# Optimization experiments

Hardware: AMD Instinct MI355X
Metric: run time of the kernel (lower is better)

Reference implementation:

```python
import jax, jax.numpy as jnp
import numpy as np

N = 50000      # nodes
E = 600000     # edges (no self-loops in data; GATConv adds them)
IN = 128       # input_dim
HID = 16       # hidden_dim
H1 = 8         # heads1
H2 = 4         # heads2
OUT = 40       # output_dim (classes)
EPS_BN = 1e-5
NEG_SLOPE = 0.2


def setup_inputs() -> dict:
    key = jax.random.key(0)
    ks = jax.random.split(key, 40)
    f32 = jnp.float32

    def p(k, shape, scale=0.1):
        return (jax.random.normal(k, shape) * scale).astype(f32)

    x = jax.random.normal(ks[0], (N, IN), f32)
    src = jax.random.randint(ks[1], (E,), 0, N)
    off = jax.random.randint(ks[2], (E,), 1, N)
    dst = (src + off) % N  # guarantees src != dst
    edge_index = jnp.stack([src, dst]).astype(jnp.int32)

    D1 = HID * H1  # 128
    D2 = HID * H2  # 64
    inp = {
        "x": x, "edge_index": edge_index,
        # conv1: IN -> HID per head, H1 heads, concat
        "W1": p(ks[3], (IN, H1 * HID)), "as1": p(ks[4], (H1, HID)), "ad1": p(ks[5], (H1, HID)), "b1": p(ks[6], (D1,)),
        "g1": jnp.ones((D1,), f32), "be1": jnp.zeros((D1,), f32),
        # conv_mid: D1 -> D1, 1 head, mean (concat=False)
        "Wm": p(ks[7], (D1, D1)), "asm": p(ks[8], (1, D1)), "adm": p(ks[9], (1, D1)), "bm": p(ks[10], (D1,)),
        "gm": jnp.ones((D1,), f32), "bem": jnp.zeros((D1,), f32),
        # conv2: D1 -> HID per head, H2 heads, concat
        "W2": p(ks[11], (D1, H2 * HID)), "as2": p(ks[12], (H2, HID)), "ad2": p(ks[13], (H2, HID)), "b2": p(ks[14], (D2,)),
        "g2": jnp.ones((D2,), f32), "be2": jnp.zeros((D2,), f32),
        # conv3: D2 -> OUT, 1 head, mean
        "W3": p(ks[15], (D2, OUT)), "as3": p(ks[16], (1, OUT)), "ad3": p(ks[17], (1, OUT)), "b3": p(ks[18], (OUT,)),
        "g3": jnp.ones((OUT,), f32), "be3": jnp.zeros((OUT,), f32),
    }
    return inp


def _gat(x, src, dst, W, a_s, a_d, b, concat):
    """PyG GATConv forward (self-loops already appended to src/dst)."""
    Nn = x.shape[0]
    H, C = a_s.shape
    h = (x @ W).reshape(Nn, H, C)                       # [N,H,C]
    s = (h * a_s).sum(-1)                               # [N,H] source score
    d = (h * a_d).sum(-1)                               # [N,H] dest score
    e = jax.nn.leaky_relu(s[src] + d[dst], NEG_SLOPE)   # [E,H]
    # segment softmax over incoming edges of each dst node
    m = jax.ops.segment_max(e, dst, num_segments=Nn)    # [N,H]
    ee = jnp.exp(e - m[dst])
    den = jax.ops.segment_sum(ee, dst, num_segments=Nn)
    alpha = ee / (den[dst] + 1e-16)                     # [E,H]
    out = jax.ops.segment_sum(h[src] * alpha[:, :, None], dst, num_segments=Nn)  # [N,H,C]
    out = out.reshape(Nn, H * C) if concat else out.mean(axis=1)
    return out + b


def _bn(x, g, b):
    mu = x.mean(axis=0)
    var = x.var(axis=0)
    return g * (x - mu) * jax.lax.rsqrt(var + EPS_BN) + b


def reference(x, edge_index, W1, as1, ad1, b1, g1, be1, Wm, asm, adm, bm, gm, bem,
              W2, as2, ad2, b2, g2, be2, W3, as3, ad3, b3, g3, be3):
    Nn = x.shape[0]
    loops = jnp.arange(Nn, dtype=edge_index.dtype)
    src = jnp.concatenate([edge_index[0], loops])
    dst = jnp.concatenate([edge_index[1], loops])

    h = jax.nn.elu(_bn(_gat(x, src, dst, W1, as1, ad1, b1, True), g1, be1))
    res = h
    h = jax.nn.elu(_bn(_gat(h, src, dst, Wm, asm, adm, bm, False), gm, bem))
    h = res + h
    h = jax.nn.elu(_bn(_gat(h, src, dst, W2, as2, ad2, b2, True), g2, be2))
    h = _bn(_gat(h, src, dst, W3, as3, ad3, b3, False), g3, be3)
    return jax.nn.log_softmax(h, axis=1)
```

## Files before the change

kernel.cpp:

```cpp
#include <hip/hip_runtime.h>
#include <hip/hip_bf16.h>
#include <math.h>

#define NN 50000
#define NE 600000
#define ET (NN + NE)

typedef __hip_bfloat16 bf16;

__global__ void k_hist(const int* __restrict__ ei, int* __restrict__ deg) {
    int e = blockIdx.x * blockDim.x + threadIdx.x;
    if (e >= ET) return;
    int d = (e < NE) ? ei[NE + e] : (e - NE);
    atomicAdd(&deg[d], 1);
}

__global__ void k_scan_local(const int* __restrict__ deg, int* __restrict__ tmp,
                             int* __restrict__ csum) {
    __shared__ int wsum[16];
    int i = blockIdx.x * 1024 + threadIdx.x;
    int lane = threadIdx.x & 63, wid = threadIdx.x >> 6;
    int x = (i < NN) ? deg[i] : 0;
    for (int off = 1; off < 64; off <<= 1) {
        int y = __shfl_up(x, off);
        if (lane >= off) x += y;
    }
    if (lane == 63) wsum[wid] = x;
    __syncthreads();
    if (wid == 0) {
        int t = (lane < 16) ? wsum[lane] : 0;
        for (int off = 1; off < 16; off <<= 1) {
            int y = __shfl_up(t, off);
            if (lane >= off) t += y;
        }
        if (lane < 16) wsum[lane] = t;
    }
    __syncthreads();
    if (wid > 0) x += wsum[wid - 1];
    if (i < NN) tmp[i] = x;
    if (threadIdx.x == 1023) csum[blockIdx.x] = x;
}

__global__ void k_scan_chunks(int* __restrict__ csum, int nchunks) {
    int lane = threadIdx.x;
    int v = (lane < nchunks) ? csum[lane] : 0;
    for (int off = 1; off < 64; off <<= 1) {
        int y = __shfl_up(v, off);
        if (lane >= off) v += y;
    }
    if (lane < nchunks) csum[lane] = v;
}

__global__ void k_rowptr(const int* __restrict__ tmp, const int* __restrict__ csum,
                         int* __restrict__ rowptr) {
    int i = blockIdx.x * blockDim.x + threadIdx.x;
    if (i == 0) rowptr[0] = 0;
    if (i < NN) {
        int chunk = i >> 10;
        int off = (chunk > 0) ? csum[chunk - 1] : 0;
        rowptr[i + 1] = tmp[i] + off;
    }
}

__global__ void k_fill(const int* __restrict__ ei, const int* __restrict__ rowptr,
                       int* __restrict__ fill, int* __restrict__ csr) {
    int e = blockIdx.x * blockDim.x + threadIdx.x;
    if (e >= ET) return;
    int s = (e < NE) ? ei[e] : (e - NE);
    int d = (e < NE) ? ei[NE + e] : (e - NE);
    int pos = atomicAdd(&fill[d], 1);
    csr[rowptr[d] + pos] = s;
}

template <int K, int D, bool FS1>
__global__ __launch_bounds__(256) void k_gemm(const float* __restrict__ X,
                                              const float* __restrict__ W,
                                              bf16* __restrict__ Hout, int nrows,
                                              const float* __restrict__ a_s,
                                              const float* __restrict__ a_d,
                                              float* __restrict__ Sout,
                                              float* __restrict__ Dvout) {
    __shared__ float Xs[64][K + 1];
    int t = threadIdx.x;
    int row0 = blockIdx.x * 64;
    for (int i = t; i < 64 * K; i += 256) {
        int r = i / K, c = i % K;
        int gr = row0 + r;
        Xs[r][c] = (gr < nrows) ? X[(size_t)gr * K + c] : 0.f;
    }
    __syncthreads();
    constexpr int DC = D / 32;
    int tx = t & 31, ty = t >> 5;
    float acc[8][DC];
#pragma unroll
    for (int r = 0; r < 8; r++)
#pragma unroll
        for (int c = 0; c < DC; c++) acc[r][c] = 0.f;
    for (int k = 0; k < K; k++) {
        float w[DC];
#pragma unroll
        for (int c = 0; c < DC; c++) w[c] = W[k * D + tx + 32 * c];
#pragma unroll
        for (int r = 0; r < 8; r++) {
            float xv = Xs[ty * 8 + r][k];
#pragma unroll
            for (int c = 0; c < DC; c++) acc[r][c] += xv * w[c];
        }
    }
#pragma unroll
    for (int r = 0; r < 8; r++) {
        int gr = row0 + ty * 8 + r;
        if (gr < nrows)
#pragma unroll
            for (int c = 0; c < DC; c++)
                Hout[(size_t)gr * D + tx + 32 * c] = __float2bfloat16(acc[r][c]);
    }
    if constexpr (FS1) {
        float asv[DC], adv[DC];
#pragma unroll
        for (int c = 0; c < DC; c++) {
            asv[c] = a_s[tx + 32 * c];
            adv[c] = a_d[tx + 32 * c];
        }
#pragma unroll
        for (int r = 0; r < 8; r++) {
            float sa = 0.f, da = 0.f;
#pragma unroll
            for (int c = 0; c < DC; c++) {
                sa += acc[r][c] * asv[c];
                da += acc[r][c] * adv[c];
            }
            for (int off = 16; off; off >>= 1) {
                sa += __shfl_xor(sa, off);
                da += __shfl_xor(da, off);
            }
            int gr = row0 + ty * 8 + r;
            if (tx == 0 && gr < nrows) {
                Sout[gr] = sa;
                Dvout[gr] = da;
            }
        }
    }
}

__global__ void k_gemm_small(const float* __restrict__ X, const float* __restrict__ W,
                             bf16* __restrict__ Hout, const float* __restrict__ a_s,
                             const float* __restrict__ a_d, float* __restrict__ S,
                             float* __restrict__ Dv) {
    __shared__ float xs[64];
    int n = blockIdx.x, t = threadIdx.x;
    xs[t] = X[n * 64 + t];
    __syncthreads();
    float acc = 0.f;
    if (t < 40) {
#pragma unroll
        for (int k = 0; k < 64; k++) acc += xs[k] * W[k * 40 + t];
        Hout[n * 40 + t] = __float2bfloat16(acc);
    }
    float sa = (t < 40) ? acc * a_s[t] : 0.f;
    float da = (t < 40) ? acc * a_d[t] : 0.f;
    for (int off = 32; off; off >>= 1) {
        sa += __shfl_xor(sa, off);
        da += __shfl_xor(da, off);
    }
    if (t == 0) {
        S[n] = sa;
        Dv[n] = da;
    }
}

template <int H, int C>
__global__ void k_scores(const bf16* __restrict__ Hb, const float* __restrict__ a_s,
                         const float* __restrict__ a_d, float* __restrict__ S,
                         float* __restrict__ Dv) {
    int t = blockIdx.x * blockDim.x + threadIdx.x;
    if (t >= NN * H) return;
    int n = t / H, h = t % H;
    const bf16* base = Hb + (size_t)n * (H * C) + h * C;
    float sa = 0.f, da = 0.f;
#pragma unroll
    for (int c = 0; c < C; c++) {
        float v = __bfloat162float(base[c]);
        sa += v * a_s[h * C + c];
        da += v * a_d[h * C + c];
    }
    S[t] = sa;
    Dv[t] = da;
}

template <int H, int C, int D>
__global__ __launch_bounds__(256) void k_aggregate(const bf16* __restrict__ Hb,
                                                   const float* __restrict__ S,
                                                   const float* __restrict__ Dv,
                                                   const int* __restrict__ rowptr,
                                                   const int* __restrict__ csr,
                                                   float* __restrict__ Out) {
    constexpr int WCAP = 64;
    __shared__ float wl[4][WCAP * H];
    int nl = threadIdx.x >> 6;
    int node = blockIdx.x * 4 + nl;
    if (node >= NN) return;
    int lane = threadIdx.x & 63;
    int r0 = rowptr[node], r1 = rowptr[node + 1];
    int cnt = r1 - r0;
    float dn[H], den[H];
#pragma unroll
    for (int h = 0; h < H; h++) {
        dn[h] = Dv[node * H + h];
        den[h] = 0.f;
    }
    for (int k = lane; k < cnt; k += 64) {
        int u = csr[r0 + k];
        float sv[H];
        if constexpr (H == 8) {
            float4 s0 = *reinterpret_cast<const float4*>(S + (size_t)u * 8);
            float4 s1 = *reinterpret_cast<const float4*>(S + (size_t)u * 8 + 4);
            sv[0] = s0.x; sv[1] = s0.y; sv[2] = s0.z; sv[3] = s0.w;
            sv[4] = s1.x; sv[5] = s1.y; sv[6] = s1.z; sv[7] = s1.w;
        } else if constexpr (H == 4) {
            float4 s0 = *reinterpret_cast<const float4*>(S + (size_t)u * 4);
            sv[0] = s0.x; sv[1] = s0.y; sv[2] = s0.z; sv[3] = s0.w;
        } else {
            sv[0] = S[u];
        }
        float ex[H];
#pragma unroll
        for (int h = 0; h < H; h++) {
            float e = sv[h] + dn[h];
            e = fmaxf(e, 0.2f * e);
            ex[h] = __expf(e);
            den[h] += ex[h];
        }
        if (k < WCAP) {
#pragma unroll
            for (int h = 0; h < H; h++) wl[nl][k * H + h] = ex[h];
        }
    }
#pragma unroll
    for (int h = 0; h < H; h++) {
        for (int off = 32; off; off >>= 1) den[h] += __shfl_xor(den[h], off);
        den[h] = 1.f / (den[h] + 1e-16f);
    }

    constexpr int EPI = (D > 64) ? 1 : 2;
    constexpr int LP = 64 / EPI;
    int sub = lane / LP;
    int j = lane % LP;
    bool act = (2 * j) < D;
    const int h_l = act ? (2 * j) / C : 0;
    float dninv_l = den[0], dn_l = dn[0];
#pragma unroll
    for (int h = 1; h < H; h++) {
        dninv_l = (h_l == h) ? den[h] : dninv_l;
        dn_l = (h_l == h) ? dn[h] : dn_l;
    }
    const float* wlp = &wl[nl][0];
    auto wof = [&](int idx, int u) -> float {
        if (idx < WCAP) return wlp[idx * H + h_l];
        float e = S[(size_t)u * H + h_l] + dn_l;
        e = fmaxf(e, 0.2f * e);
        return __expf(e);
    };
    float ax = 0.f, ay = 0.f;
    int k = sub;
    for (; k + 3 * EPI < cnt; k += 4 * EPI) {
        int u0 = csr[r0 + k];
        int u1 = csr[r0 + k + EPI];
        int u2 = csr[r0 + k + 2 * EPI];
        int u3 = csr[r0 + k + 3 * EPI];
        unsigned p0 = 0, p1 = 0, p2 = 0, p3 = 0;
        if (act) {
            p0 = *reinterpret_cast<const unsigned*>(Hb + (size_t)u0 * D + 2 * j);
            p1 = *reinterpret_cast<const unsigned*>(Hb + (size_t)u1 * D + 2 * j);
            p2 = *reinterpret_cast<const unsigned*>(Hb + (size_t)u2 * D + 2 * j);
            p3 = *reinterpret_cast<const unsigned*>(Hb + (size_t)u3 * D + 2 * j);
        }
        float w0 = wof(k, u0), w1 = wof(k + EPI, u1);
        float w2 = wof(k + 2 * EPI, u2), w3 = wof(k + 3 * EPI, u3);
        ax += w0 * __uint_as_float(p0 << 16) + w1 * __uint_as_float(p1 << 16) +
              w2 * __uint_as_float(p2 << 16) + w3 * __uint_as_float(p3 << 16);
        ay += w0 * __uint_as_float(p0 & 0xffff0000u) + w1 * __uint_as_float(p1 & 0xffff0000u) +
              w2 * __uint_as_float(p2 & 0xffff0000u) + w3 * __uint_as_float(p3 & 0xffff0000u);
    }
    for (; k < cnt; k += EPI) {
        int u = csr[r0 + k];
        unsigned pv = 0;
        if (act) pv = *reinterpret_cast<const unsigned*>(Hb + (size_t)u * D + 2 * j);
        float w = wof(k, u);
        ax += w * __uint_as_float(pv << 16);
        ay += w * __uint_as_float(pv & 0xffff0000u);
    }
    if (EPI == 2) {
        ax += __shfl_xor(ax, 32);
        ay += __shfl_xor(ay, 32);
    }
    if (act && lane < LP) {
        *reinterpret_cast<float2*>(Out + (size_t)node * D + 2 * j) =
            make_float2(ax * dninv_l, ay * dninv_l);
    }
}

template <int D>
__global__ void k_bnstats(const float* __restrict__ X, float* __restrict__ colsum,
                          float* __restrict__ colsq) {
    int col = threadIdx.x;
    if (col >= D) return;
    float s = 0.f, q = 0.f;
    for (int r = blockIdx.x; r < NN; r += gridDim.x) {
        float v = X[(size_t)r * D + col];
        s += v;
        q += v * v;
    }
    atomicAdd(&colsum[col], s);
    atomicAdd(&colsq[col], q);
}

template <int D, int MODE>
__global__ void k_bnapply(const float* __restrict__ X, const float* __restrict__ colsum,
                          const float* __restrict__ colsq, const float* __restrict__ g,
                          const float* __restrict__ be, const float* __restrict__ res,
                          float* __restrict__ Out) {
    int idx = blockIdx.x * blockDim.x + threadIdx.x;
    if (idx >= NN * D) return;
    int col = idx % D;
    float mu = colsum[col] * (1.f / NN);
    float var = colsq[col] * (1.f / NN) - mu * mu;
    float sc = g[col] * rsqrtf(var + 1e-5f);
    float v = sc * (X[idx] - mu) + be[col];
    v = (v > 0.f) ? v : (__expf(v) - 1.f);
    if (MODE == 1) v += res[idx];
    Out[idx] = v;
}

__global__ void k_bn_logsoftmax(const float* __restrict__ X, const float* __restrict__ colsum,
                                const float* __restrict__ colsq, const float* __restrict__ g,
                                const float* __restrict__ be, float* __restrict__ Out) {
    int node = (blockIdx.x * blockDim.x + threadIdx.x) >> 6;
    int lane = threadIdx.x & 63;
    if (node >= NN) return;
    float bnv = 0.f, v = -1e30f;
    if (lane < 40) {
        float mu = colsum[lane] * (1.f / NN);
        float var = colsq[lane] * (1.f / NN) - mu * mu;
        float sc = g[lane] * rsqrtf(var + 1e-5f);
        bnv = sc * (X[node * 40 + lane] - mu) + be[lane];
        v = bnv;
    }
    float m = v;
    for (int off = 32; off; off >>= 1) m = fmaxf(m, __shfl_xor(m, off));
    float ex = (lane < 40) ? expf(bnv - m) : 0.f;
    for (int off = 32; off; off >>= 1) ex += __shfl_xor(ex, off);
    float lse = m + logf(ex);
    if (lane < 40) Out[node * 40 + lane] = bnv - lse;
}

extern "C" void kernel_launch(void* const* d_in, const int* in_sizes, int n_in,
                              void* d_out, int out_size, void* d_ws, size_t ws_size,
                              hipStream_t stream) {
    (void)in_sizes; (void)n_in; (void)out_size; (void)ws_size;
    const float* x   = (const float*)d_in[0];
    const int*   ei  = (const int*)d_in[1];
    const float* W1  = (const float*)d_in[2];
    const float* as1 = (const float*)d_in[3];
    const float* ad1 = (const float*)d_in[4];
    const float* g1  = (const float*)d_in[6];
    const float* be1 = (const float*)d_in[7];
    const float* Wm  = (const float*)d_in[8];
    const float* asm_ = (const float*)d_in[9];
    const float* adm = (const float*)d_in[10];
    const float* gm  = (const float*)d_in[12];
    const float* bem = (const float*)d_in[13];
    const float* W2  = (const float*)d_in[14];
    const float* as2 = (const float*)d_in[15];
    const float* ad2 = (const float*)d_in[16];
    const float* g2  = (const float*)d_in[18];
    const float* be2 = (const float*)d_in[19];
    const float* W3  = (const float*)d_in[20];
    const float* as3 = (const float*)d_in[21];
    const float* ad3 = (const float*)d_in[22];
    const float* g3  = (const float*)d_in[24];
    const float* be3 = (const float*)d_in[25];
    float* out = (float*)d_out;

    char* ws = (char*)d_ws;
    size_t off = 0;
    auto alloc = [&](size_t b) {
        void* p = ws + off;
        off = (off + b + 255) & ~(size_t)255;
        return p;
    };
    int* rowptr = (int*)alloc((NN + 1) * 4);
    int* csr    = (int*)alloc((size_t)ET * 4);
    int* deg    = (int*)alloc(NN * 4);
    int* tmp    = (int*)alloc(NN * 4);
    int* csum   = (int*)alloc(256 * 4);
    bf16* Hbf   = (bf16*)alloc((size_t)NN * 128 * 2);
    float* A    = (float*)alloc((size_t)NN * 128 * 4);
    float* B    = (float*)alloc((size_t)NN * 128 * 4);
    float* S    = (float*)alloc((size_t)NN * 8 * 4);
    float* Dv   = (float*)alloc((size_t)NN * 8 * 4);
    float* cs   = (float*)alloc(256 * 4);
    float* cq   = cs + 128;

    const int nchunks = (NN + 1023) / 1024;

    hipMemsetAsync(deg, 0, NN * 4, stream);
    k_hist<<<(ET + 255) / 256, 256, 0, stream>>>(ei, deg);
    k_scan_local<<<nchunks, 1024, 0, stream>>>(deg, tmp, csum);
    k_scan_chunks<<<1, 64, 0, stream>>>(csum, nchunks);
    k_rowptr<<<(NN + 255) / 256, 256, 0, stream>>>(tmp, csum, rowptr);
    hipMemsetAsync(deg, 0, NN * 4, stream);
    k_fill<<<(ET + 255) / 256, 256, 0, stream>>>(ei, rowptr, deg, csr);

    const int gemm_blocks = (NN + 63) / 64;
    const int node_wave_blocks = (NN + 3) / 4;

    k_gemm<128, 128, false><<<gemm_blocks, 256, 0, stream>>>(x, W1, Hbf, NN, nullptr, nullptr, nullptr, nullptr);
    k_scores<8, 16><<<(NN * 8 + 255) / 256, 256, 0, stream>>>(Hbf, as1, ad1, S, Dv);
    k_aggregate<8, 16, 128><<<node_wave_blocks, 256, 0, stream>>>(Hbf, S, Dv, rowptr, csr, A);
    hipMemsetAsync(cs, 0, 256 * 4, stream);
    k_bnstats<128><<<512, 128, 0, stream>>>(A, cs, cq);
    k_bnapply<128, 0><<<(NN * 128 + 255) / 256, 256, 0, stream>>>(A, cs, cq, g1, be1, nullptr, B);

    k_gemm<128, 128, true><<<gemm_blocks, 256, 0, stream>>>(B, Wm, Hbf, NN, asm_, adm, S, Dv);
    k_aggregate<1, 128, 128><<<node_wave_blocks, 256, 0, stream>>>(Hbf, S, Dv, rowptr, csr, A);
    hipMemsetAsync(cs, 0, 256 * 4, stream);
    k_bnstats<128><<<512, 128, 0, stream>>>(A, cs, cq);
    k_bnapply<128, 1><<<(NN * 128 + 255) / 256, 256, 0, stream>>>(A, cs, cq, gm, bem, B, A);

    k_gemm<128, 64, false><<<gemm_blocks, 256, 0, stream>>>(A, W2, Hbf, NN, nullptr, nullptr, nullptr, nullptr);
    k_scores<4, 16><<<(NN * 4 + 255) / 256, 256, 0, stream>>>(Hbf, as2, ad2, S, Dv);
    k_aggregate<4, 16, 64><<<node_wave_blocks, 256, 0, stream>>>(Hbf, S, Dv, rowptr, csr, B);
    hipMemsetAsync(cs, 0, 256 * 4, stream);
    k_bnstats<64><<<512, 64, 0, stream>>>(B, cs, cq);
    k_bnapply<64, 0><<<(NN * 64 + 255) / 256, 256, 0, stream>>>(B, cs, cq, g2, be2, nullptr, B);

    k_gemm_small<<<NN, 64, 0, stream>>>(B, W3, Hbf, as3, ad3, S, Dv);
    k_aggregate<1, 40, 40><<<node_wave_blocks, 256, 0, stream>>>(Hbf, S, Dv, rowptr, csr, A);
    hipMemsetAsync(cs, 0, 256 * 4, stream);
    k_bnstats<40><<<512, 64, 0, stream>>>(A, cs, cq);
    k_bn_logsoftmax<<<node_wave_blocks, 256, 0, stream>>>(A, cs, cq, g3, be3, out);
}
```

Baseline: 673.1 us.

## Replace FP32 SIMT GEMMs with bf16 MFMA kernels and fuse score computation

Swaps the three shared-memory FP32 GEMMs for a one-wavefront-per-16-rows kernel using the 16x16x32 bf16 MFMA instruction. Weights are pre-transposed and converted to bf16 by a small kernel, and activations are converted to bf16 on load. The attention source and destination scores are computed from the accumulators inside the GEMM epilogue, which removes the separate k_scores passes. In exchange, inputs now go through the GEMM in bf16 instead of fp32, and the kernel assumes NN is divisible by 16.

```diff
diff --git a/kernel.cpp b/kernel.cpp
--- a/kernel.cpp
+++ b/kernel.cpp
@@ -7,6 +7,14 @@
 #define ET (NN + NE)
 
 typedef __hip_bfloat16 bf16;
+typedef __attribute__((ext_vector_type(8))) short bf16x8;
+typedef __attribute__((ext_vector_type(4))) float f32x4;
+
+static __device__ inline unsigned short f2bf(float f) {
+    union { __hip_bfloat16 h; unsigned short u; } v;
+    v.h = __float2bfloat16(f);
+    return v.u;
+}
 
 __global__ void k_hist(const int* __restrict__ ei, int* __restrict__ deg) {
     int e = blockIdx.x * blockDim.x + threadIdx.x;
@@ -72,72 +80,83 @@
     csr[rowptr[d] + pos] = s;
 }
 
-template <int K, int D, bool FS1>
-__global__ __launch_bounds__(256) void k_gemm(const float* __restrict__ X,
-                                              const float* __restrict__ W,
-                                              bf16* __restrict__ Hout, int nrows,
-                                              const float* __restrict__ a_s,
-                                              const float* __restrict__ a_d,
-                                              float* __restrict__ Sout,
-                                              float* __restrict__ Dvout) {
-    __shared__ float Xs[64][K + 1];
-    int t = threadIdx.x;
-    int row0 = blockIdx.x * 64;
-    for (int i = t; i < 64 * K; i += 256) {
-        int r = i / K, c = i % K;
-        int gr = row0 + r;
-        Xs[r][c] = (gr < nrows) ? X[(size_t)gr * K + c] : 0.f;
-    }
-    __syncthreads();
-    constexpr int DC = D / 32;
-    int tx = t & 31, ty = t >> 5;
-    float acc[8][DC];
-#pragma unroll
-    for (int r = 0; r < 8; r++)
-#pragma unroll
-        for (int c = 0; c < DC; c++) acc[r][c] = 0.f;
-    for (int k = 0; k < K; k++) {
-        float w[DC];
-#pragma unroll
-        for (int c = 0; c < DC; c++) w[c] = W[k * D + tx + 32 * c];
-#pragma unroll
-        for (int r = 0; r < 8; r++) {
-            float xv = Xs[ty * 8 + r][k];
-#pragma unroll
-            for (int c = 0; c < DC; c++) acc[r][c] += xv * w[c];
-        }
-    }
-#pragma unroll
-    for (int r = 0; r < 8; r++) {
-        int gr = row0 + ty * 8 + r;
-        if (gr < nrows)
-#pragma unroll
-            for (int c = 0; c < DC; c++)
-                Hout[(size_t)gr * D + tx + 32 * c] = __float2bfloat16(acc[r][c]);
-    }
-    if constexpr (FS1) {
-        float asv[DC], adv[DC];
-#pragma unroll
-        for (int c = 0; c < DC; c++) {
-            asv[c] = a_s[tx + 32 * c];
-            adv[c] = a_d[tx + 32 * c];
-        }
-#pragma unroll
-        for (int r = 0; r < 8; r++) {
+template <int K, int D>
+__global__ void k_wconv(const float* __restrict__ W, short* __restrict__ WT) {
+    int idx = blockIdx.x * 256 + threadIdx.x;
+    if (idx >= K * D) return;
+    int d = idx / K, k = idx % K;
+    WT[idx] = (short)f2bf(W[k * D + d]);
+}
+
+template <int D, int HF>
+__global__ __launch_bounds__(64) void k_gemm_mfma(const float* __restrict__ X,
+                                                  const short* __restrict__ WT,
+                                                  bf16* __restrict__ Hout,
+                                                  const float* __restrict__ a_s,
+                                                  const float* __restrict__ a_d,
+                                                  float* __restrict__ S,
+                                                  float* __restrict__ Dv) {
+    constexpr int K = 128;
+    constexpr int NT = D / 16;
+    int lane = threadIdx.x;
+    int rb = blockIdx.x * 16;
+    int m = lane & 15, kg = lane >> 4;
+
+    f32x4 acc[NT];
+#pragma unroll
+    for (int n = 0; n < NT; n++) acc[n] = (f32x4){0.f, 0.f, 0.f, 0.f};
+
+    const float* xp = X + (size_t)(rb + m) * K + kg * 8;
+#pragma unroll
+    for (int k0 = 0; k0 < K; k0 += 32) {
+        float4 f0 = *reinterpret_cast<const float4*>(xp + k0);
+        float4 f1 = *reinterpret_cast<const float4*>(xp + k0 + 4);
+        bf16x8 a;
+        a[0] = (short)f2bf(f0.x); a[1] = (short)f2bf(f0.y);
+        a[2] = (short)f2bf(f0.z); a[3] = (short)f2bf(f0.w);
+        a[4] = (short)f2bf(f1.x); a[5] = (short)f2bf(f1.y);
+        a[6] = (short)f2bf(f1.z); a[7] = (short)f2bf(f1.w);
+#pragma unroll
+        for (int n = 0; n < NT; n++) {
+            bf16x8 b = *reinterpret_cast<const bf16x8*>(WT + (size_t)(n * 16 + m) * K + k0 + kg * 8);
+            acc[n] = __builtin_amdgcn_mfma_f32_16x16x32_bf16(a, b, acc[n], 0, 0, 0);
+        }
+    }
+
+    float asv[NT], adv[NT];
+#pragma unroll
+    for (int n = 0; n < NT; n++) {
+        asv[n] = a_s[n * 16 + m];
+        adv[n] = a_d[n * 16 + m];
+    }
+#pragma unroll
+    for (int r = 0; r < 4; r++) {
+        int row = rb + kg * 4 + r;
+#pragma unroll
+        for (int n = 0; n < NT; n++)
+            Hout[(size_t)row * D + n * 16 + m] = __float2bfloat16(acc[n][r]);
+        if constexpr (HF == 1) {
             float sa = 0.f, da = 0.f;
 #pragma unroll
-            for (int c = 0; c < DC; c++) {
-                sa += acc[r][c] * asv[c];
-                da += acc[r][c] * adv[c];
+            for (int n = 0; n < NT; n++) {
+                sa += acc[n][r] * asv[n];
+                da += acc[n][r] * adv[n];
             }
-            for (int off = 16; off; off >>= 1) {
+            for (int off = 1; off < 16; off <<= 1) {
                 sa += __shfl_xor(sa, off);
                 da += __shfl_xor(da, off);
             }
-            int gr = row0 + ty * 8 + r;
-            if (tx == 0 && gr < nrows) {
-                Sout[gr] = sa;
-                Dvout[gr] = da;
+            if (m == 0) { S[row] = sa; Dv[row] = da; }
+        } else {
+#pragma unroll
+            for (int n = 0; n < NT; n++) {
+                float sa = acc[n][r] * asv[n];
+                float da = acc[n][r] * adv[n];
+                for (int off = 1; off < 16; off <<= 1) {
+                    sa += __shfl_xor(sa, off);
+                    da += __shfl_xor(da, off);
+                }
+                if (m == 0) { S[row * HF + n] = sa; Dv[row * HF + n] = da; }
             }
         }
     }
@@ -167,25 +186,6 @@
         S[n] = sa;
         Dv[n] = da;
     }
-}
-
-template <int H, int C>
-__global__ void k_scores(const bf16* __restrict__ Hb, const float* __restrict__ a_s,
-                         const float* __restrict__ a_d, float* __restrict__ S,
-                         float* __restrict__ Dv) {
-    int t = blockIdx.x * blockDim.x + threadIdx.x;
-    if (t >= NN * H) return;
-    int n = t / H, h = t % H;
-    const bf16* base = Hb + (size_t)n * (H * C) + h * C;
-    float sa = 0.f, da = 0.f;
-#pragma unroll
-    for (int c = 0; c < C; c++) {
-        float v = __bfloat162float(base[c]);
-        sa += v * a_s[h * C + c];
-        da += v * a_d[h * C + c];
-    }
-    S[t] = sa;
-    Dv[t] = da;
 }
 
 template <int H, int C, int D>
@@ -401,8 +401,15 @@
     float* Dv   = (float*)alloc((size_t)NN * 8 * 4);
     float* cs   = (float*)alloc(256 * 4);
     float* cq   = cs + 128;
+    short* WT1  = (short*)alloc(128 * 128 * 2);
+    short* WTm  = (short*)alloc(128 * 128 * 2);
+    short* WT2  = (short*)alloc(128 * 64 * 2);
 
     const int nchunks = (NN + 1023) / 1024;
+
+    k_wconv<128, 128><<<64, 256, 0, stream>>>(W1, WT1);
+    k_wconv<128, 128><<<64, 256, 0, stream>>>(Wm, WTm);
+    k_wconv<128, 64><<<32, 256, 0, stream>>>(W2, WT2);
 
     hipMemsetAsync(deg, 0, NN * 4, stream);
     k_hist<<<(ET + 255) / 256, 256, 0, stream>>>(ei, deg);
@@ -412,24 +419,22 @@
     hipMemsetAsync(deg, 0, NN * 4, stream);
     k_fill<<<(ET + 255) / 256, 256, 0, stream>>>(ei, rowptr, deg, csr);
 
-    const int gemm_blocks = (NN + 63) / 64;
+    const int mfma_blocks = NN / 16;
     const int node_wave_blocks = (NN + 3) / 4;
 
-    k_gemm<128, 128, false><<<gemm_blocks, 256, 0, stream>>>(x, W1, Hbf, NN, nullptr, nullptr, nullptr, nullptr);
-    k_scores<8, 16><<<(NN * 8 + 255) / 256, 256, 0, stream>>>(Hbf, as1, ad1, S, Dv);
+    k_gemm_mfma<128, 8><<<mfma_blocks, 64, 0, stream>>>(x, WT1, Hbf, as1, ad1, S, Dv);
     k_aggregate<8, 16, 128><<<node_wave_blocks, 256, 0, stream>>>(Hbf, S, Dv, rowptr, csr, A);
     hipMemsetAsync(cs, 0, 256 * 4, stream);
     k_bnstats<128><<<512, 128, 0, stream>>>(A, cs, cq);
     k_bnapply<128, 0><<<(NN * 128 + 255) / 256, 256, 0, stream>>>(A, cs, cq, g1, be1, nullptr, B);
 
-    k_gemm<128, 128, true><<<gemm_blocks, 256, 0, stream>>>(B, Wm, Hbf, NN, asm_, adm, S, Dv);
+    k_gemm_mfma<128, 1><<<mfma_blocks, 64, 0, stream>>>(B, WTm, Hbf, asm_, adm, S, Dv);
     k_aggregate<1, 128, 128><<<node_wave_blocks, 256, 0, stream>>>(Hbf, S, Dv, rowptr, csr, A);
     hipMemsetAsync(cs, 0, 256 * 4, stream);
     k_bnstats<128><<<512, 128, 0, stream>>>(A, cs, cq);
     k_bnapply<128, 1><<<(NN * 128 + 255) / 256, 256, 0, stream>>>(A, cs, cq, gm, bem, B, A);
 
-    k_gemm<128, 64, false><<<gemm_blocks, 256, 0, stream>>>(A, W2, Hbf, NN, nullptr, nullptr, nullptr, nullptr);
-    k_scores<4, 16><<<(NN * 4 + 255) / 256, 256, 0, stream>>>(Hbf, as2, ad2, S, Dv);
+    k_gemm_mfma<64, 4><<<mfma_blocks, 64, 0, stream>>>(A, WT2, Hbf, as2, ad2, S, Dv);
     k_aggregate<4, 16, 64><<<node_wave_blocks, 256, 0, stream>>>(Hbf, S, Dv, rowptr, csr, B);
     hipMemsetAsync(cs, 0, 256 * 4, stream);
     k_bnstats<64><<<512, 64, 0, stream>>>(B, cs, cq);
```

After: 624.9 us. 7.2% less time.
